# Kernel optimization log

Hardware: AMD Instinct MI355X
Metric: run time of the kernel (lower is better)

The kernel has to match this reference:

```python
import jax, jax.numpy as jnp
import numpy as np

SIGS = (0.08, 0.02)  # hardcoded sigmas from Varifold_loss.__init__
EPS = 1e-12


def _face_geom(V, F):
    # V: [nv,3] float, F: [nf,3] int -> centers [nf,3], areas [nf], unit normals [nf,3]
    v0, v1, v2 = V[F[:, 0]], V[F[:, 1]], V[F[:, 2]]
    C = (v0 + v1 + v2) / 3.0
    N = 0.5 * jnp.cross(v1 - v0, v2 - v0)  # area-weighted normal
    L = jnp.sqrt(jnp.sum(N * N, axis=-1) + EPS)  # triangle area
    return C, L, N / L[:, None]


def _inner(Cx, Lx, Nx, Cy, Ly, Ny, sigma):
    # unoriented squared-dot Gaussian varifold inner product: sum_ij Lx_i Ly_j exp(-|c_i-c_j|^2/s^2) (n_i.n_j)^2
    d2 = (Cx * Cx).sum(-1)[:, None] + (Cy * Cy).sum(-1)[None, :] - 2.0 * (Cx @ Cy.T)
    K = jnp.exp(-d2 / (sigma * sigma)) * (Nx @ Ny.T) ** 2  # [nfx, nfy]
    return Lx @ (K @ Ly)


def setup_inputs() -> dict:
    key = jax.random.key(0)
    k1, k2, k3, k4 = jax.random.split(key, 4)
    B, V, F = 1, 5023, 8000
    return {
        "predictions": jax.random.normal(k1, (B, V, 3), jnp.float32) * 0.1,
        "targets": jax.random.normal(k2, (B, V, 3), jnp.float32) * 0.1,
        "pred_faces": jax.random.randint(k3, (B, F, 3), 0, V),
        "target_faces": jax.random.randint(k4, (B, F, 3), 0, V),
    }


def reference(predictions, targets, pred_faces, target_faces):
    def per_item(V1, F1, V2, F2):
        C1, L1, N1 = _face_geom(V1, F1)
        C2, L2, N2 = _face_geom(V2, F2)
        total = jnp.float32(0.0)
        for s in SIGS:  # small fixed set of sigmas (structural loop)
            w = jnp.float32((s / SIGS[0]) ** 2)
            total = total + w * (
                _inner(C1, L1, N1, C1, L1, N1, s)
                + _inner(C2, L2, N2, C2, L2, N2, s)
                - 2.0 * _inner(C1, L1, N1, C2, L2, N2, s)
            )
        return total
    L = jax.vmap(per_item)(predictions, pred_faces, targets, target_faces)
    return jnp.mean(L)
```

## Files before the change

### kernel.cpp

```cpp
#include <hip/hip_runtime.h>

#define GBLOCK 256
#define BLOCK 256
#define TILE 128
#define LN2 0.69314718055994530942
#define K1F ((float)(-1.0 / (0.08 * 0.08 * LN2)))
#define W2F 0.0625f

typedef __attribute__((ext_vector_type(8))) short short8;
typedef __attribute__((ext_vector_type(4))) float f32x4;

__device__ __forceinline__ ushort btr(float x) {
    return (ushort)(__builtin_bit_cast(unsigned, x) >> 16);
}
__device__ __forceinline__ float bfl(ushort h) {
    return __builtin_bit_cast(float, ((unsigned)h) << 16);
}
__device__ __forceinline__ unsigned pk2(ushort a, ushort b) {
    return (unsigned)a | ((unsigned)b << 16);
}


__global__ void geom_kernel(const float* __restrict__ vpred,
                            const float* __restrict__ vtarg,
                            const int* __restrict__ pf,
                            const int* __restrict__ tf,
                            ushort* __restrict__ ttA, ushort* __restrict__ ttB,
                            ushort* __restrict__ ndA, ushort* __restrict__ ndB,
                            float* __restrict__ partials, int F, int Fpad)
{
    int id = blockIdx.x * blockDim.x + threadIdx.x;
    float diag = 0.0f;
    if (id < 2 * Fpad) {
        int m = (id >= Fpad) ? 1 : 0;
        int f = id - m * Fpad;
        ushort chh[3] = {0, 0, 0}, cll[3] = {0, 0, 0};
        ushort mhh[3] = {0, 0, 0}, mll[3] = {0, 0, 0};
        ushort s1h = 0, s1l = 0, ONE = 0;
        if (f < F) {
            const float* Vv = m ? vtarg : vpred;
            const int* Fc = m ? tf : pf;
            int i0 = Fc[3 * f + 0];
            int i1 = Fc[3 * f + 1];
            int i2 = Fc[3 * f + 2];
            float ax = Vv[3 * i0 + 0], ay = Vv[3 * i0 + 1], az = Vv[3 * i0 + 2];
            float bx = Vv[3 * i1 + 0], by = Vv[3 * i1 + 1], bz = Vv[3 * i1 + 2];
            float cx = Vv[3 * i2 + 0], cy = Vv[3 * i2 + 1], cz = Vv[3 * i2 + 2];

            const float third = 1.0f / 3.0f;
            float Cx = (ax + bx + cx) * third;
            float Cy = (ay + by + cy) * third;
            float Cz = (az + bz + cz) * third;

            float e1x = bx - ax, e1y = by - ay, e1z = bz - az;
            float e2x = cx - ax, e2y = cy - ay, e2z = cz - az;
            float Nx = 0.5f * (e1y * e2z - e1z * e2y);
            float Ny = 0.5f * (e1z * e2x - e1x * e2z);
            float Nz = 0.5f * (e1x * e2y - e1y * e2x);
            float nn = Nx * Nx + Ny * Ny + Nz * Nz;
            float L = sqrtf(nn + 1e-12f);
            float invSL = 1.0f / sqrtf(L);

            const float g = sqrtf(-2.0f * K1F);
            float cc[3] = {g * Cx, g * Cy, g * Cz};
            float M[3] = {Nx * invSL, Ny * invSL, Nz * invSL};
            float s1 = K1F * (Cx * Cx + Cy * Cy + Cz * Cz);
#pragma unroll
            for (int d = 0; d < 3; ++d) {
                chh[d] = btr(cc[d]);
                cll[d] = btr(cc[d] - bfl(chh[d]));
                mhh[d] = btr(M[d]);
                mll[d] = btr(M[d] - bfl(mhh[d]));
            }
            s1h = btr(s1);
            s1l = btr(s1 - bfl(s1h));
            ONE = 0x3F80;

            float d = nn / L;
            diag = (1.0f + W2F) * d * d;
        }
        size_t base = (size_t)id * 32;
        uint4 z4 = {0u, 0u, 0u, 0u};
        uint4 q0, q1;
        q0.x = pk2(chh[0], chh[1]); q0.y = pk2(chh[2], chh[0]);
        q0.z = pk2(chh[1], chh[2]); q0.w = pk2(cll[0], cll[1]);
        q1.x = pk2(cll[2], s1h);    q1.y = pk2(s1l, ONE);
        q1.z = pk2(ONE, 0);         q1.w = 0u;
        { uint4* p = (uint4*)(ttA + base); p[0] = q0; p[1] = q1; p[2] = z4; p[3] = z4; }
        q0.x = pk2(chh[0], chh[1]); q0.y = pk2(chh[2], cll[0]);
        q0.z = pk2(cll[1], cll[2]); q0.w = pk2(chh[0], chh[1]);
        q1.x = pk2(chh[2], ONE);    q1.y = pk2(ONE, s1h);
        q1.z = pk2(s1l, 0);         q1.w = 0u;
        { uint4* p = (uint4*)(ttB + base); p[0] = q0; p[1] = q1; p[2] = z4; p[3] = z4; }
        q0.x = pk2(mhh[0], mhh[1]); q0.y = pk2(mhh[2], mhh[0]);
        q0.z = pk2(mhh[1], mhh[2]); q0.w = pk2(mll[0], mll[1]);
        q1.x = pk2(mll[2], 0);      q1.y = 0u; q1.z = 0u; q1.w = 0u;
        { uint4* p = (uint4*)(ndA + base); p[0] = q0; p[1] = q1; p[2] = z4; p[3] = z4; }
        q0.x = pk2(mhh[0], mhh[1]); q0.y = pk2(mhh[2], mll[0]);
        q0.z = pk2(mll[1], mll[2]); q0.w = pk2(mhh[0], mhh[1]);
        q1.x = pk2(mhh[2], 0);      q1.y = 0u; q1.z = 0u; q1.w = 0u;
        { uint4* p = (uint4*)(ndB + base); p[0] = q0; p[1] = q1; p[2] = z4; p[3] = z4; }
    }
    for (int off = 32; off > 0; off >>= 1) diag += __shfl_down(diag, off, 64);
    int wid = threadIdx.x >> 6;
    if ((threadIdx.x & 63) == 0)
        partials[blockIdx.x * (GBLOCK / 64) + wid] = diag;
}

#define MLOOP(PRED)                                                          \
    for (int jt = 0; jt < 8; ++jt) {                                         \
        int rowB = jbase + jt * 16 + l15;                                    \
        short8 btt = *(const short8*)(tB + (size_t)rowB * 32 + koff);        \
        short8 bnd = *(const short8*)(nB + (size_t)rowB * 32 + koff);        \
        _Pragma("unroll")                                                    \
        for (int s = 0; s < 2; ++s) {                                        \
            f32x4 zz = {0.f, 0.f, 0.f, 0.f};                                 \
            f32x4 Dt = __builtin_amdgcn_mfma_f32_16x16x32_bf16(              \
                attF[s], btt, zz, 0, 0, 0);                                  \
            f32x4 Dn = __builtin_amdgcn_mfma_f32_16x16x32_bf16(              \
                andF[s], bnd, zz, 0, 0, 0);                                  \
            _Pragma("unroll")                                                \
            for (int r = 0; r < 4; ++r) {                                    \
                float nd = Dn[r];                                            \
                float p = nd * nd;                                           \
                if (PRED) {                                                  \
                    int ii = ibase + s * 16 + kg * 4 + r;                    \
                    int jj = jbase + jt * 16 + l15;                          \
                    p = (jj < ii) ? p : 0.0f;                                \
                }                                                            \
                float e1 = __builtin_amdgcn_exp2f(Dt[r]);                    \
                float u1 = e1 * e1;                                          \
                float u2 = u1 * u1;                                          \
                float u3 = u2 * u2;                                          \
                float e2 = u3 * u3;                                          \
                accA = fmaf(p, e1, accA);                                    \
                accB = fmaf(p, e2, accB);                                    \
            }                                                                \
        }                                                                    \
    }

__launch_bounds__(BLOCK, 8)
__global__ void pair_kernel(const ushort* __restrict__ ttA,
                            const ushort* __restrict__ ttB,
                            const ushort* __restrict__ ndA,
                            const ushort* __restrict__ ndB,
                            float* __restrict__ partials,
                            int Fpad, int nJC, int nSym)
{
    int bid = blockIdx.x;
    int t, ib, jc;
    bool pred = false;
    if (bid < 2 * nSym) {
        t = (bid < nSym) ? 0 : 1;
        int r = bid - t * nSym;
        int off = 0, ibf = 0;
        for (;;) {
            int c = ibf + 1;
            if (c > nJC) c = nJC;
            if (r < off + c) break;
            off += c;
            ibf++;
        }
        ib = ibf;
        jc = r - off;
        pred = (jc >= ib);
    } else {
        int r = bid - 2 * nSym;
        t = 2;
        ib = r / nJC;
        jc = r - ib * nJC;
    }
    float coeff = (t == 2) ? -2.0f : 2.0f;
    int X = (t == 1) ? 1 : 0;
    int Y = (t == 0) ? 0 : 1;

    int tid = threadIdx.x, wid = tid >> 6, lane = tid & 63;
    int l15 = lane & 15, kg = lane >> 4;
    int koff = kg * 8;

    const ushort* tA = ttA + (size_t)X * Fpad * 32;
    const ushort* nA = ndA + (size_t)X * Fpad * 32;
    const ushort* tB = ttB + (size_t)Y * Fpad * 32;
    const ushort* nB = ndB + (size_t)Y * Fpad * 32;

    int ibase = ib * TILE + wid * 32;
    int jbase = jc * TILE;
    int rowA0 = ibase + l15;

    short8 attF[2], andF[2];
    attF[0] = *(const short8*)(tA + (size_t)rowA0 * 32 + koff);
    attF[1] = *(const short8*)(tA + (size_t)(rowA0 + 16) * 32 + koff);
    andF[0] = *(const short8*)(nA + (size_t)rowA0 * 32 + koff);
    andF[1] = *(const short8*)(nA + (size_t)(rowA0 + 16) * 32 + koff);

    float accA = 0.0f, accB = 0.0f;

    if (!pred) {
        MLOOP(false)
    } else {
        MLOOP(true)
    }

    float ps = coeff * fmaf(W2F, accB, accA);
    for (int off = 32; off > 0; off >>= 1) ps += __shfl_down(ps, off, 64);
    __shared__ float wsum[BLOCK / 64];
    if (lane == 0) wsum[wid] = ps;
    __syncthreads();
    if (tid == 0)
        partials[bid] = wsum[0] + wsum[1] + wsum[2] + wsum[3];
}

__global__ void final_reduce(const float* __restrict__ partials, int n,
                             float* __restrict__ out)
{
    float s = 0.0f;
    for (int i = threadIdx.x; i < n; i += GBLOCK) s += partials[i];
    for (int off = 32; off > 0; off >>= 1) s += __shfl_down(s, off, 64);
    __shared__ float wsum[GBLOCK / 64];
    int wid = threadIdx.x >> 6;
    if ((threadIdx.x & 63) == 0) wsum[wid] = s;
    __syncthreads();
    if (threadIdx.x == 0)
        out[0] = wsum[0] + wsum[1] + wsum[2] + wsum[3];
}

extern "C" void kernel_launch(void* const* d_in, const int* in_sizes, int n_in,
                              void* d_out, int out_size, void* d_ws, size_t ws_size,
                              hipStream_t stream) {
    const float* vpred = (const float*)d_in[0];
    const float* vtarg = (const float*)d_in[1];
    const int* pf = (const int*)d_in[2];
    const int* tf = (const int*)d_in[3];
    float* out = (float*)d_out;

    int F = in_sizes[2] / 3;
    int nIB = (F + TILE - 1) / TILE;
    int Fpad = nIB * TILE;
    int nJC = nIB;
    int nSym = nIB * (nIB + 1) / 2;
    int pairBlocks = 2 * nSym + nIB * nJC;

    size_t sz1 = (size_t)2 * Fpad * 32 * sizeof(ushort);
    char* w = (char*)d_ws;
    ushort* ttA = (ushort*)(w);
    ushort* ttB = (ushort*)(w + sz1);
    ushort* ndA = (ushort*)(w + 2 * sz1);
    ushort* ndB = (ushort*)(w + 3 * sz1);
    float* partials = (float*)(w + 4 * sz1);

    int gblocks = (2 * Fpad + GBLOCK - 1) / GBLOCK;
    int geomSlots = gblocks * (GBLOCK / 64);

    geom_kernel<<<gblocks, GBLOCK, 0, stream>>>(
        vpred, vtarg, pf, tf, ttA, ttB, ndA, ndB, partials, F, Fpad);

    pair_kernel<<<pairBlocks, BLOCK, 0, stream>>>(
        ttA, ttB, ndA, ndB, partials + geomSlots, Fpad, nJC, nSym);

    final_reduce<<<1, GBLOCK, 0, stream>>>(
        partials, geomSlots + pairBlocks, out);
}
```

Measured before the change: 114.9 us.

## Switch pair kernel to 32x32x16 bf16 MFMA with halved K padding

Replaces the 16x16x32 bf16 MFMA tiles with 32x32x16 MFMA, so the padded K dimension shrinks from 32 to 16 and the per-face feature rows are half as large. Each wave now computes a 32x32 block per instruction, with one A fragment per wave and 32-row B loads. The geometry kernel writes the compact 16-element layout and drops the zero-padding stores. The second exponential is now a separate exp2 of 16x the argument instead of four repeated squarings, which trades multiplies for extra transcendental-unit work.

```diff
diff --git a/kernel.cpp b/kernel.cpp
--- a/kernel.cpp
+++ b/kernel.cpp
@@ -8,7 +8,7 @@
 #define W2F 0.0625f
 
 typedef __attribute__((ext_vector_type(8))) short short8;
-typedef __attribute__((ext_vector_type(4))) float f32x4;
+typedef __attribute__((ext_vector_type(16))) float f32x16;
 
 __device__ __forceinline__ ushort btr(float x) {
     return (ushort)(__builtin_bit_cast(unsigned, x) >> 16);
@@ -79,27 +79,26 @@
             float d = nn / L;
             diag = (1.0f + W2F) * d * d;
         }
-        size_t base = (size_t)id * 32;
-        uint4 z4 = {0u, 0u, 0u, 0u};
+        size_t base = (size_t)id * 16;
         uint4 q0, q1;
         q0.x = pk2(chh[0], chh[1]); q0.y = pk2(chh[2], chh[0]);
         q0.z = pk2(chh[1], chh[2]); q0.w = pk2(cll[0], cll[1]);
         q1.x = pk2(cll[2], s1h);    q1.y = pk2(s1l, ONE);
         q1.z = pk2(ONE, 0);         q1.w = 0u;
-        { uint4* p = (uint4*)(ttA + base); p[0] = q0; p[1] = q1; p[2] = z4; p[3] = z4; }
+        { uint4* p = (uint4*)(ttA + base); p[0] = q0; p[1] = q1; }
         q0.x = pk2(chh[0], chh[1]); q0.y = pk2(chh[2], cll[0]);
         q0.z = pk2(cll[1], cll[2]); q0.w = pk2(chh[0], chh[1]);
         q1.x = pk2(chh[2], ONE);    q1.y = pk2(ONE, s1h);
         q1.z = pk2(s1l, 0);         q1.w = 0u;
-        { uint4* p = (uint4*)(ttB + base); p[0] = q0; p[1] = q1; p[2] = z4; p[3] = z4; }
+        { uint4* p = (uint4*)(ttB + base); p[0] = q0; p[1] = q1; }
         q0.x = pk2(mhh[0], mhh[1]); q0.y = pk2(mhh[2], mhh[0]);
         q0.z = pk2(mhh[1], mhh[2]); q0.w = pk2(mll[0], mll[1]);
         q1.x = pk2(mll[2], 0);      q1.y = 0u; q1.z = 0u; q1.w = 0u;
-        { uint4* p = (uint4*)(ndA + base); p[0] = q0; p[1] = q1; p[2] = z4; p[3] = z4; }
+        { uint4* p = (uint4*)(ndA + base); p[0] = q0; p[1] = q1; }
         q0.x = pk2(mhh[0], mhh[1]); q0.y = pk2(mhh[2], mll[0]);
         q0.z = pk2(mll[1], mll[2]); q0.w = pk2(mhh[0], mhh[1]);
         q1.x = pk2(mhh[2], 0);      q1.y = 0u; q1.z = 0u; q1.w = 0u;
-        { uint4* p = (uint4*)(ndB + base); p[0] = q0; p[1] = q1; p[2] = z4; p[3] = z4; }
+        { uint4* p = (uint4*)(ndB + base); p[0] = q0; p[1] = q1; }
     }
     for (int off = 32; off > 0; off >>= 1) diag += __shfl_down(diag, off, 64);
     int wid = threadIdx.x >> 6;
@@ -108,34 +107,27 @@
 }
 
 #define MLOOP(PRED)                                                          \
-    for (int jt = 0; jt < 8; ++jt) {                                         \
-        int rowB = jbase + jt * 16 + l15;                                    \
-        short8 btt = *(const short8*)(tB + (size_t)rowB * 32 + koff);        \
-        short8 bnd = *(const short8*)(nB + (size_t)rowB * 32 + koff);        \
+    for (int js = 0; js < 4; ++js) {                                         \
+        int rowB = jbase + js * 32 + l31;                                    \
+        short8 btt = *(const short8*)(tB + (size_t)rowB * 16 + koff);        \
+        short8 bnd = *(const short8*)(nB + (size_t)rowB * 16 + koff);        \
+        f32x16 Dt = __builtin_amdgcn_mfma_f32_32x32x16_bf16(                 \
+            attF, btt, zz, 0, 0, 0);                                         \
+        f32x16 Dn = __builtin_amdgcn_mfma_f32_32x32x16_bf16(                 \
+            andF, bnd, zz, 0, 0, 0);                                         \
         _Pragma("unroll")                                                    \
-        for (int s = 0; s < 2; ++s) {                                        \
-            f32x4 zz = {0.f, 0.f, 0.f, 0.f};                                 \
-            f32x4 Dt = __builtin_amdgcn_mfma_f32_16x16x32_bf16(              \
-                attF[s], btt, zz, 0, 0, 0);                                  \
-            f32x4 Dn = __builtin_amdgcn_mfma_f32_16x16x32_bf16(              \
-                andF[s], bnd, zz, 0, 0, 0);                                  \
-            _Pragma("unroll")                                                \
-            for (int r = 0; r < 4; ++r) {                                    \
-                float nd = Dn[r];                                            \
-                float p = nd * nd;                                           \
-                if (PRED) {                                                  \
-                    int ii = ibase + s * 16 + kg * 4 + r;                    \
-                    int jj = jbase + jt * 16 + l15;                          \
-                    p = (jj < ii) ? p : 0.0f;                                \
-                }                                                            \
-                float e1 = __builtin_amdgcn_exp2f(Dt[r]);                    \
-                float u1 = e1 * e1;                                          \
-                float u2 = u1 * u1;                                          \
-                float u3 = u2 * u2;                                          \
-                float e2 = u3 * u3;                                          \
-                accA = fmaf(p, e1, accA);                                    \
-                accB = fmaf(p, e2, accB);                                    \
+        for (int r = 0; r < 16; ++r) {                                       \
+            float nd = Dn[r];                                                \
+            float p = nd * nd;                                               \
+            if (PRED) {                                                      \
+                int ii = ibase + (r & 3) + 8 * (r >> 2) + 4 * kh;            \
+                int jj = jbase + js * 32 + l31;                              \
+                p = (jj < ii) ? p : 0.0f;                                    \
             }                                                                \
+            float e1 = __builtin_amdgcn_exp2f(Dt[r]);                        \
+            float e2 = __builtin_amdgcn_exp2f(Dt[r] * 16.0f);                \
+            accA = fmaf(p, e1, accA);                                        \
+            accB = fmaf(p, e2, accB);                                        \
         }                                                                    \
     }
 
@@ -175,24 +167,23 @@
     int Y = (t == 0) ? 0 : 1;
 
     int tid = threadIdx.x, wid = tid >> 6, lane = tid & 63;
-    int l15 = lane & 15, kg = lane >> 4;
-    int koff = kg * 8;
-
-    const ushort* tA = ttA + (size_t)X * Fpad * 32;
-    const ushort* nA = ndA + (size_t)X * Fpad * 32;
-    const ushort* tB = ttB + (size_t)Y * Fpad * 32;
-    const ushort* nB = ndB + (size_t)Y * Fpad * 32;
+    int l31 = lane & 31, kh = lane >> 5;
+    int koff = kh * 8;
+
+    const ushort* tA = ttA + (size_t)X * Fpad * 16;
+    const ushort* nA = ndA + (size_t)X * Fpad * 16;
+    const ushort* tB = ttB + (size_t)Y * Fpad * 16;
+    const ushort* nB = ndB + (size_t)Y * Fpad * 16;
 
     int ibase = ib * TILE + wid * 32;
     int jbase = jc * TILE;
-    int rowA0 = ibase + l15;
-
-    short8 attF[2], andF[2];
-    attF[0] = *(const short8*)(tA + (size_t)rowA0 * 32 + koff);
-    attF[1] = *(const short8*)(tA + (size_t)(rowA0 + 16) * 32 + koff);
-    andF[0] = *(const short8*)(nA + (size_t)rowA0 * 32 + koff);
-    andF[1] = *(const short8*)(nA + (size_t)(rowA0 + 16) * 32 + koff);
-
+    int rowA = ibase + l31;
+
+    short8 attF = *(const short8*)(tA + (size_t)rowA * 16 + koff);
+    short8 andF = *(const short8*)(nA + (size_t)rowA * 16 + koff);
+
+    const f32x16 zz = {0.f, 0.f, 0.f, 0.f, 0.f, 0.f, 0.f, 0.f,
+                       0.f, 0.f, 0.f, 0.f, 0.f, 0.f, 0.f, 0.f};
     float accA = 0.0f, accB = 0.0f;
 
     if (!pred) {
@@ -240,7 +231,7 @@
     int nSym = nIB * (nIB + 1) / 2;
     int pairBlocks = 2 * nSym + nIB * nJC;
 
-    size_t sz1 = (size_t)2 * Fpad * 32 * sizeof(ushort);
+    size_t sz1 = (size_t)2 * Fpad * 16 * sizeof(ushort);
     char* w = (char*)d_ws;
     ushort* ttA = (ushort*)(w);
     ushort* ttB = (ushort*)(w + sz1);
```

Result: slower. 177.0 us (+54.0%).
